# Kernel optimization log

Measured on AMD Instinct MI355X. Metric: run time of the kernel, lower is better.

## Reference

```python
import jax, jax.numpy as jnp
import numpy as np

EPS = 1e-9
NUM_CLASSES = 10


def setup_inputs() -> dict:
    key = jax.random.key(0)
    k1, k2, k3, k4 = jax.random.split(key, 4)
    B, N, D = 1024, 16384, 512
    bound = 1.0 / (D ** 0.5)
    return {
        "x": jax.random.normal(k1, (B, D), dtype=jnp.float32),
        "ex_feats": jax.random.normal(k2, (N, D), dtype=jnp.float32),
        "ex_labels": jax.random.randint(k3, (N,), 0, NUM_CLASSES),
        "w_unconstrained": jax.random.uniform(k4, (D,), dtype=jnp.float32, minval=-bound, maxval=bound),
        "gamma_unconstrained": jnp.asarray(1.0, dtype=jnp.float32),
        "beta_unconstrained": jnp.asarray(1.0, dtype=jnp.float32),
    }


def reference(x, ex_feats, ex_labels, w_unconstrained, gamma_unconstrained, beta_unconstrained):
    # Constrained parameters
    beta = jax.nn.softplus(beta_unconstrained) + EPS      # scalar
    gamma = jax.nn.softplus(gamma_unconstrained) + EPS    # scalar
    w = jax.nn.softmax(w_unconstrained) + EPS             # (D,), positive, ~sums to 1

    # Weighted squared distance via quadratic (GEMM) expansion:
    # d[b,n] = sum_k w_k * (x[b,k] - e[n,k])^2
    #        = (x^2 @ w)[b] + (e^2 @ w)[n] - 2 * ((x*w) @ e^T)[b,n]
    x2w = (x * x) @ w                                     # (B,)
    e2w = (ex_feats * ex_feats) @ w                       # (N,)
    cross = (x * w[None, :]) @ ex_feats.T                 # (B, N) GEMM
    d = x2w[:, None] + e2w[None, :] - 2.0 * cross         # (B, N)

    sim = jnp.exp(-beta * d)                              # (B, N)

    # Scatter-add sim by class label -> class_sum (B, C).
    # With small C this is a dense GEMM against a one-hot matrix.
    onehot = jax.nn.one_hot(ex_labels, NUM_CLASSES, dtype=sim.dtype)  # (N, C)
    class_sum = sim @ onehot                              # (B, C)

    logits = gamma * jnp.log(class_sum + EPS)
    return logits
```

## Files before the change

### kernel.cpp

```cpp
#include <hip/hip_runtime.h>
#include <hip/hip_bf16.h>
#include <cstdint>


typedef __attribute__((ext_vector_type(4))) float f32x4;
typedef __attribute__((ext_vector_type(8))) __bf16 bf16x8;
typedef __attribute__((ext_vector_type(4))) _Float16 half4;
typedef __attribute__((ext_vector_type(4))) unsigned int u32x4;

#define DDIM 512
#define NC 10
#define NCP 16
#define NECH 64
#define EPSF 1e-9f

__device__ inline float wave_sum(float v) {
  #pragma unroll
  for (int o = 32; o > 0; o >>= 1) v += __shfl_xor(v, o, 64);
  return v;
}

__device__ inline float softplus(float x) {
  return (x > 20.0f) ? x : log1pf(__expf(x));
}

__device__ inline unsigned cvtpk(float lo, float hi) {
  unsigned r;
  asm("v_cvt_pk_bf16_f32 %0, %1, %2" : "=v"(r) : "v"(lo), "v"(hi));
  return r;
}

__global__ __launch_bounds__(512, 2) void gemm_mega(
    const float* __restrict__ x, const float* __restrict__ ex,
    const int* __restrict__ labels, const float* __restrict__ wu,
    const float* __restrict__ bu, float* __restrict__ part) {
  __shared__ __attribute__((aligned(16))) unsigned short smem[2 * 16384];
  __shared__ float wlds[512];
  __shared__ float sm[16];
  __shared__ float e2l[256];
  __shared__ float x2l[256];
  __shared__ int lab[256];
  const int tid = threadIdx.x, lane = tid & 63, wid = tid >> 6;

  const int orig = blockIdx.x;
  const int xcd = orig & 7;
  const int local = orig >> 3;
  const int be = xcd * 8 + (local >> 2);
  const int bb = local & 3;

  if (tid < 256) lab[tid] = labels[be * 256 + tid];

  {
    float v = wu[tid];
    float m = v;
    #pragma unroll
    for (int o = 32; o > 0; o >>= 1) m = fmaxf(m, __shfl_xor(m, o, 64));
    if (lane == 0) sm[wid] = m;
    __syncthreads();
    float mm = sm[0];
    #pragma unroll
    for (int i = 1; i < 8; ++i) mm = fmaxf(mm, sm[i]);
    float e = __expf(v - mm);
    float s = wave_sum(e);
    if (lane == 0) sm[8 + wid] = s;
    __syncthreads();
    float ss = 0.f;
    #pragma unroll
    for (int i = 0; i < 8; ++i) ss += sm[8 + i];
    wlds[tid] = e / ss + EPSF;
    __syncthreads();
  }

  const int srow = tid >> 2;
  const int kc = (tid & 3) ^ (srow & 3);
  const float* eP0 = ex + (size_t)(be * 256 + srow) * DDIM + kc * 8;
  const float* eP1 = eP0 + (size_t)128 * DDIM;
  const float* xP0 = x + (size_t)(bb * 256 + srow) * DDIM + kc * 8;
  const float* xP1 = xP0 + (size_t)128 * DDIM;
  const int dE0 = tid * 8,           dE1 = (512 + tid) * 8;
  const int dX0 = 8192 + tid * 8,    dX1 = 8192 + (512 + tid) * 8;

  float e2a0 = 0.f, e2a1 = 0.f, x2a0 = 0.f, x2a1 = 0.f;

  const int WE = (wid >> 2) * 128;
  const int WB = (wid & 3) * 64;
  int eoff[8], xoff[4];
  {
    const int ch = lane >> 4;
    #pragma unroll
    for (int f = 0; f < 8; ++f) {
      int er = WE + f * 16 + (lane & 15);
      eoff[f] = er * 64 + ((ch ^ (er & 3)) * 16);
    }
    #pragma unroll
    for (int f = 0; f < 4; ++f) {
      int xr = WB + f * 16 + (lane & 15);
      xoff[f] = 16384 + xr * 64 + ((ch ^ (xr & 3)) * 16);
    }
  }

  float4 sE0a, sE0b, sE1a, sE1b, sX0a, sX0b, sX1a, sX1b;

#define ISSUE(KT) do {                                                  \
    const float* p0 = eP0 + (KT) * 32;                                  \
    const float* p1 = eP1 + (KT) * 32;                                  \
    const float* p2 = xP0 + (KT) * 32;                                  \
    const float* p3 = xP1 + (KT) * 32;                                  \
    sE0a = *(const float4*)p0; sE0b = *(const float4*)(p0 + 4);         \
    sE1a = *(const float4*)p1; sE1b = *(const float4*)(p1 + 4);         \
    sX0a = *(const float4*)p2; sX0b = *(const float4*)(p2 + 4);         \
    sX1a = *(const float4*)p3; sX1b = *(const float4*)(p3 + 4);         \
  } while (0)

#define CVTSTORE(KT, BUFS) do {                                         \
    const float4 w0 = *(const float4*)&wlds[(KT) * 32 + kc * 8];        \
    const float4 w1 = *(const float4*)&wlds[(KT) * 32 + kc * 8 + 4];    \
    u32x4 pk;                                                           \
    pk[0] = cvtpk(sE0a.x, sE0a.y); pk[1] = cvtpk(sE0a.z, sE0a.w);       \
    pk[2] = cvtpk(sE0b.x, sE0b.y); pk[3] = cvtpk(sE0b.z, sE0b.w);       \
    e2a0 += sE0a.x*sE0a.x*w0.x + sE0a.y*sE0a.y*w0.y                     \
          + sE0a.z*sE0a.z*w0.z + sE0a.w*sE0a.w*w0.w                     \
          + sE0b.x*sE0b.x*w1.x + sE0b.y*sE0b.y*w1.y                     \
          + sE0b.z*sE0b.z*w1.z + sE0b.w*sE0b.w*w1.w;                    \
    *(u32x4*)&smem[(BUFS) + dE0] = pk;                                  \
    pk[0] = cvtpk(sE1a.x, sE1a.y); pk[1] = cvtpk(sE1a.z, sE1a.w);       \
    pk[2] = cvtpk(sE1b.x, sE1b.y); pk[3] = cvtpk(sE1b.z, sE1b.w);       \
    e2a1 += sE1a.x*sE1a.x*w0.x + sE1a.y*sE1a.y*w0.y                     \
          + sE1a.z*sE1a.z*w0.z + sE1a.w*sE1a.w*w0.w                     \
          + sE1b.x*sE1b.x*w1.x + sE1b.y*sE1b.y*w1.y                     \
          + sE1b.z*sE1b.z*w1.z + sE1b.w*sE1b.w*w1.w;                    \
    *(u32x4*)&smem[(BUFS) + dE1] = pk;                                  \
    float a0 = sX0a.x*w0.x, a1 = sX0a.y*w0.y, a2 = sX0a.z*w0.z,         \
          a3 = sX0a.w*w0.w, a4 = sX0b.x*w1.x, a5 = sX0b.y*w1.y,         \
          a6 = sX0b.z*w1.z, a7 = sX0b.w*w1.w;                           \
    pk[0] = cvtpk(a0, a1); pk[1] = cvtpk(a2, a3);                       \
    pk[2] = cvtpk(a4, a5); pk[3] = cvtpk(a6, a7);                       \
    x2a0 += a0*sX0a.x + a1*sX0a.y + a2*sX0a.z + a3*sX0a.w               \
          + a4*sX0b.x + a5*sX0b.y + a6*sX0b.z + a7*sX0b.w;              \
    *(u32x4*)&smem[(BUFS) + dX0] = pk;                                  \
    a0 = sX1a.x*w0.x; a1 = sX1a.y*w0.y; a2 = sX1a.z*w0.z;               \
    a3 = sX1a.w*w0.w; a4 = sX1b.x*w1.x; a5 = sX1b.y*w1.y;               \
    a6 = sX1b.z*w1.z; a7 = sX1b.w*w1.w;                                 \
    pk[0] = cvtpk(a0, a1); pk[1] = cvtpk(a2, a3);                       \
    pk[2] = cvtpk(a4, a5); pk[3] = cvtpk(a6, a7);                       \
    x2a1 += a0*sX1a.x + a1*sX1a.y + a2*sX1a.z + a3*sX1a.w               \
          + a4*sX1b.x + a5*sX1b.y + a6*sX1b.z + a7*sX1b.w;              \
    *(u32x4*)&smem[(BUFS) + dX1] = pk;                                  \
  } while (0)

  ISSUE(0);
  CVTSTORE(0, 0);
  __syncthreads();

  f32x4 acc[8][4] = {};
  for (int kt = 0; kt < 16; ++kt) {
    const int cur = kt & 1;
    if (kt < 15) ISSUE(kt + 1);
    const char* base = (const char*)smem + cur * 32768;
    bf16x8 ef[8], xf[4];
    #pragma unroll
    for (int f = 0; f < 8; ++f) ef[f] = *(const bf16x8*)(base + eoff[f]);
    #pragma unroll
    for (int f = 0; f < 4; ++f) xf[f] = *(const bf16x8*)(base + xoff[f]);
    #pragma unroll
    for (int fe = 0; fe < 8; ++fe)
      #pragma unroll
      for (int fb = 0; fb < 4; ++fb)
        acc[fe][fb] = __builtin_amdgcn_mfma_f32_16x16x32_bf16(ef[fe], xf[fb], acc[fe][fb], 0, 0, 0);
    if (kt < 15) CVTSTORE(kt + 1, (cur ^ 1) * 16384);
    __syncthreads();
  }
#undef ISSUE
#undef CVTSTORE

  e2a0 += __shfl_xor(e2a0, 1, 64); e2a0 += __shfl_xor(e2a0, 2, 64);
  e2a1 += __shfl_xor(e2a1, 1, 64); e2a1 += __shfl_xor(e2a1, 2, 64);
  x2a0 += __shfl_xor(x2a0, 1, 64); x2a0 += __shfl_xor(x2a0, 2, 64);
  x2a1 += __shfl_xor(x2a1, 1, 64); x2a1 += __shfl_xor(x2a1, 2, 64);
  if ((tid & 3) == 0) {
    e2l[srow] = e2a0; e2l[srow + 128] = e2a1;
    x2l[srow] = x2a0; x2l[srow + 128] = x2a1;
  }
  __syncthreads();

  const float beta = softplus(bu[0]) + EPSF;
  const int rb = (lane >> 4) * 4;
  const int col = lane & 15;
  float e2v[8][4];
  #pragma unroll
  for (int fe = 0; fe < 8; ++fe)
    #pragma unroll
    for (int r = 0; r < 4; ++r)
      e2v[fe][r] = e2l[WE + fe * 16 + rb + r];
  half4 oh[8];
  #pragma unroll
  for (int fe = 0; fe < 8; ++fe)
    #pragma unroll
    for (int i = 0; i < 4; ++i)
      oh[fe][i] = (lab[WE + fe * 16 + rb + i] == col) ? (_Float16)1.0f : (_Float16)0.0f;

  f32x4 csv[4];
  #pragma unroll
  for (int fb = 0; fb < 4; ++fb) {
    const float xv = x2l[WB + fb * 16 + col];
    f32x4 cs = {0.f, 0.f, 0.f, 0.f};
    #pragma unroll
    for (int fe = 0; fe < 8; ++fe) {
      half4 sa;
      #pragma unroll
      for (int r = 0; r < 4; ++r)
        sa[r] = (_Float16)__expf(-beta * (xv + e2v[fe][r] - 2.0f * acc[fe][fb][r]));
      cs = __builtin_amdgcn_mfma_f32_16x16x16f16(sa, oh[fe], cs, 0, 0, 0);
    }
    csv[fb] = cs;
  }

  float* red = (float*)smem;
  const int half = WE >> 7;
  #pragma unroll
  for (int fb = 0; fb < 4; ++fb)
    #pragma unroll
    for (int r = 0; r < 4; ++r)
      red[(((half << 8) | (WB + fb * 16 + rb + r)) << 4) | col] = csv[fb][r];
  __syncthreads();

  {
    const int o = tid * 8;
    const int rl = o >> 4;
    const int c0 = o & 15;
    const float4* p0 = (const float4*)&red[(rl << 4) | c0];
    const float4* p1 = (const float4*)&red[((256 | rl) << 4) | c0];
    float4 a0 = p0[0], a1 = p0[1], b0 = p1[0], b1 = p1[1];
    float4 r0 = {a0.x + b0.x, a0.y + b0.y, a0.z + b0.z, a0.w + b0.w};
    float4 r1 = {a1.x + b1.x, a1.y + b1.y, a1.z + b1.z, a1.w + b1.w};
    float* g = &part[(((size_t)(bb * 256 + rl)) * NECH + be) * NCP + c0];
    *(float4*)g = r0;
    *(float4*)(g + 4) = r1;
  }
}

__global__ __launch_bounds__(256) void reduce_logits(
    const float* __restrict__ part, const float* __restrict__ gu,
    float* __restrict__ out) {
  const int lane = threadIdx.x & 63, wd = threadIdx.x >> 6;
  const int b = blockIdx.x * 4 + wd;
  const int cl = lane & 15, ch0 = lane >> 4;
  const float* p = part + (size_t)b * NECH * NCP;
  float v = 0.f;
  #pragma unroll
  for (int k = 0; k < 16; ++k)
    v += p[(ch0 + 4 * k) * NCP + cl];
  v += __shfl_xor(v, 16, 64);
  v += __shfl_xor(v, 32, 64);
  if (lane < NC) {
    const float gamma = softplus(gu[0]) + EPSF;
    out[b * NC + lane] = gamma * logf(v + EPSF);
  }
}

extern "C" void kernel_launch(void* const* d_in, const int* in_sizes, int n_in,
                              void* d_out, int out_size, void* d_ws, size_t ws_size,
                              hipStream_t stream) {
  const float* x  = (const float*)d_in[0];
  const float* ex = (const float*)d_in[1];
  const int* labels = (const int*)d_in[2];
  const float* wu = (const float*)d_in[3];
  const float* gu = (const float*)d_in[4];
  const float* bu = (const float*)d_in[5];
  float* out = (float*)d_out;
  const int B = in_sizes[0] / DDIM;
  const int N = in_sizes[2];

  float* part = (float*)d_ws;
  const size_t need = (size_t)B * NECH * NCP * 4;
  if (ws_size < need) return;

  gemm_mega<<<(N / 256) * (B / 256), 512, 0, stream>>>(x, ex, labels, wu, bu, part);
  reduce_logits<<<B / 4, 256, 0, stream>>>(part, gu, out);
}
```

Before: 39.94 us.

## Double block to 1024 threads and halve per-wave GEMM tile

Each block now runs 16 waves instead of 8. Each wave computes a 64x64 slice of the 256x256 tile instead of 128x64, and each thread stages one row chunk per operand instead of two. The aim is more latency hiding and lower per-thread register pressure. The LDS swizzle changes to XOR on (row>>1)&3. The final class-sum reduction now combines four partial quadrants instead of two. The launch bound of (1024,4) requests a very aggressive register budget, which may cause spills, and per-wave MFMA reuse of LDS fragments drops.

```diff
diff --git a/kernel.cpp b/kernel.cpp
--- a/kernel.cpp
+++ b/kernel.cpp
@@ -14,12 +14,6 @@
 #define NECH 64
 #define EPSF 1e-9f
 
-__device__ inline float wave_sum(float v) {
-  #pragma unroll
-  for (int o = 32; o > 0; o >>= 1) v += __shfl_xor(v, o, 64);
-  return v;
-}
-
 __device__ inline float softplus(float x) {
   return (x > 20.0f) ? x : log1pf(__expf(x));
 }
@@ -30,7 +24,7 @@
   return r;
 }
 
-__global__ __launch_bounds__(512, 2) void gemm_mega(
+__global__ __launch_bounds__(1024, 4) void gemm_mega(
     const float* __restrict__ x, const float* __restrict__ ex,
     const int* __restrict__ labels, const float* __restrict__ wu,
     const float* __restrict__ bu, float* __restrict__ part) {
@@ -50,7 +44,7 @@
 
   if (tid < 256) lab[tid] = labels[be * 256 + tid];
 
-  {
+  if (tid < 512) {
     float v = wu[tid];
     float m = v;
     #pragma unroll
@@ -61,109 +55,91 @@
     #pragma unroll
     for (int i = 1; i < 8; ++i) mm = fmaxf(mm, sm[i]);
     float e = __expf(v - mm);
-    float s = wave_sum(e);
+    float s = e;
+    #pragma unroll
+    for (int o = 32; o > 0; o >>= 1) s += __shfl_xor(s, o, 64);
     if (lane == 0) sm[8 + wid] = s;
     __syncthreads();
     float ss = 0.f;
     #pragma unroll
     for (int i = 0; i < 8; ++i) ss += sm[8 + i];
     wlds[tid] = e / ss + EPSF;
-    __syncthreads();
-  }
+  } else {
+    __syncthreads();
+    __syncthreads();
+  }
+  __syncthreads();
 
   const int srow = tid >> 2;
-  const int kc = (tid & 3) ^ (srow & 3);
-  const float* eP0 = ex + (size_t)(be * 256 + srow) * DDIM + kc * 8;
-  const float* eP1 = eP0 + (size_t)128 * DDIM;
-  const float* xP0 = x + (size_t)(bb * 256 + srow) * DDIM + kc * 8;
-  const float* xP1 = xP0 + (size_t)128 * DDIM;
-  const int dE0 = tid * 8,           dE1 = (512 + tid) * 8;
-  const int dX0 = 8192 + tid * 8,    dX1 = 8192 + (512 + tid) * 8;
-
-  float e2a0 = 0.f, e2a1 = 0.f, x2a0 = 0.f, x2a1 = 0.f;
-
-  const int WE = (wid >> 2) * 128;
+  const int kc = (tid & 3) ^ ((srow >> 1) & 3);
+  const float* eP = ex + (size_t)(be * 256 + srow) * DDIM + kc * 8;
+  const float* xP = x + (size_t)(bb * 256 + srow) * DDIM + kc * 8;
+  const int dE = tid * 8;
+  const int dX = 8192 + tid * 8;
+
+  float e2a = 0.f, x2a = 0.f;
+
+  const int WE = (wid >> 2) * 64;
   const int WB = (wid & 3) * 64;
-  int eoff[8], xoff[4];
+  int eoff[4], xoff[4];
   {
     const int ch = lane >> 4;
     #pragma unroll
-    for (int f = 0; f < 8; ++f) {
+    for (int f = 0; f < 4; ++f) {
       int er = WE + f * 16 + (lane & 15);
-      eoff[f] = er * 64 + ((ch ^ (er & 3)) * 16);
+      eoff[f] = er * 64 + ((ch ^ ((er >> 1) & 3)) * 16);
+      int xr = WB + f * 16 + (lane & 15);
+      xoff[f] = 16384 + xr * 64 + ((ch ^ ((xr >> 1) & 3)) * 16);
     }
-    #pragma unroll
-    for (int f = 0; f < 4; ++f) {
-      int xr = WB + f * 16 + (lane & 15);
-      xoff[f] = 16384 + xr * 64 + ((ch ^ (xr & 3)) * 16);
-    }
-  }
-
-  float4 sE0a, sE0b, sE1a, sE1b, sX0a, sX0b, sX1a, sX1b;
+  }
+
+  float4 sEa, sEb, sXa, sXb;
 
 #define ISSUE(KT) do {                                                  \
-    const float* p0 = eP0 + (KT) * 32;                                  \
-    const float* p1 = eP1 + (KT) * 32;                                  \
-    const float* p2 = xP0 + (KT) * 32;                                  \
-    const float* p3 = xP1 + (KT) * 32;                                  \
-    sE0a = *(const float4*)p0; sE0b = *(const float4*)(p0 + 4);         \
-    sE1a = *(const float4*)p1; sE1b = *(const float4*)(p1 + 4);         \
-    sX0a = *(const float4*)p2; sX0b = *(const float4*)(p2 + 4);         \
-    sX1a = *(const float4*)p3; sX1b = *(const float4*)(p3 + 4);         \
+    const float* p0 = eP + (KT) * 32;                                   \
+    const float* p1 = xP + (KT) * 32;                                   \
+    sEa = *(const float4*)p0; sEb = *(const float4*)(p0 + 4);           \
+    sXa = *(const float4*)p1; sXb = *(const float4*)(p1 + 4);           \
   } while (0)
 
 #define CVTSTORE(KT, BUFS) do {                                         \
     const float4 w0 = *(const float4*)&wlds[(KT) * 32 + kc * 8];        \
     const float4 w1 = *(const float4*)&wlds[(KT) * 32 + kc * 8 + 4];    \
     u32x4 pk;                                                           \
-    pk[0] = cvtpk(sE0a.x, sE0a.y); pk[1] = cvtpk(sE0a.z, sE0a.w);       \
-    pk[2] = cvtpk(sE0b.x, sE0b.y); pk[3] = cvtpk(sE0b.z, sE0b.w);       \
-    e2a0 += sE0a.x*sE0a.x*w0.x + sE0a.y*sE0a.y*w0.y                     \
-          + sE0a.z*sE0a.z*w0.z + sE0a.w*sE0a.w*w0.w                     \
-          + sE0b.x*sE0b.x*w1.x + sE0b.y*sE0b.y*w1.y                     \
-          + sE0b.z*sE0b.z*w1.z + sE0b.w*sE0b.w*w1.w;                    \
-    *(u32x4*)&smem[(BUFS) + dE0] = pk;                                  \
-    pk[0] = cvtpk(sE1a.x, sE1a.y); pk[1] = cvtpk(sE1a.z, sE1a.w);       \
-    pk[2] = cvtpk(sE1b.x, sE1b.y); pk[3] = cvtpk(sE1b.z, sE1b.w);       \
-    e2a1 += sE1a.x*sE1a.x*w0.x + sE1a.y*sE1a.y*w0.y                     \
-          + sE1a.z*sE1a.z*w0.z + sE1a.w*sE1a.w*w0.w                     \
-          + sE1b.x*sE1b.x*w1.x + sE1b.y*sE1b.y*w1.y                     \
-          + sE1b.z*sE1b.z*w1.z + sE1b.w*sE1b.w*w1.w;                    \
-    *(u32x4*)&smem[(BUFS) + dE1] = pk;                                  \
-    float a0 = sX0a.x*w0.x, a1 = sX0a.y*w0.y, a2 = sX0a.z*w0.z,         \
-          a3 = sX0a.w*w0.w, a4 = sX0b.x*w1.x, a5 = sX0b.y*w1.y,         \
-          a6 = sX0b.z*w1.z, a7 = sX0b.w*w1.w;                           \
+    pk[0] = cvtpk(sEa.x, sEa.y); pk[1] = cvtpk(sEa.z, sEa.w);           \
+    pk[2] = cvtpk(sEb.x, sEb.y); pk[3] = cvtpk(sEb.z, sEb.w);           \
+    e2a += sEa.x*sEa.x*w0.x + sEa.y*sEa.y*w0.y                          \
+         + sEa.z*sEa.z*w0.z + sEa.w*sEa.w*w0.w                          \
+         + sEb.x*sEb.x*w1.x + sEb.y*sEb.y*w1.y                          \
+         + sEb.z*sEb.z*w1.z + sEb.w*sEb.w*w1.w;                         \
+    *(u32x4*)&smem[(BUFS) + dE] = pk;                                   \
+    float a0 = sXa.x*w0.x, a1 = sXa.y*w0.y, a2 = sXa.z*w0.z,            \
+          a3 = sXa.w*w0.w, a4 = sXb.x*w1.x, a5 = sXb.y*w1.y,            \
+          a6 = sXb.z*w1.z, a7 = sXb.w*w1.w;                             \
     pk[0] = cvtpk(a0, a1); pk[1] = cvtpk(a2, a3);                       \
     pk[2] = cvtpk(a4, a5); pk[3] = cvtpk(a6, a7);                       \
-    x2a0 += a0*sX0a.x + a1*sX0a.y + a2*sX0a.z + a3*sX0a.w               \
-          + a4*sX0b.x + a5*sX0b.y + a6*sX0b.z + a7*sX0b.w;              \
-    *(u32x4*)&smem[(BUFS) + dX0] = pk;                                  \
-    a0 = sX1a.x*w0.x; a1 = sX1a.y*w0.y; a2 = sX1a.z*w0.z;               \
-    a3 = sX1a.w*w0.w; a4 = sX1b.x*w1.x; a5 = sX1b.y*w1.y;               \
-    a6 = sX1b.z*w1.z; a7 = sX1b.w*w1.w;                                 \
-    pk[0] = cvtpk(a0, a1); pk[1] = cvtpk(a2, a3);                       \
-    pk[2] = cvtpk(a4, a5); pk[3] = cvtpk(a6, a7);                       \
-    x2a1 += a0*sX1a.x + a1*sX1a.y + a2*sX1a.z + a3*sX1a.w               \
-          + a4*sX1b.x + a5*sX1b.y + a6*sX1b.z + a7*sX1b.w;              \
-    *(u32x4*)&smem[(BUFS) + dX1] = pk;                                  \
+    x2a += a0*sXa.x + a1*sXa.y + a2*sXa.z + a3*sXa.w                    \
+         + a4*sXb.x + a5*sXb.y + a6*sXb.z + a7*sXb.w;                   \
+    *(u32x4*)&smem[(BUFS) + dX] = pk;                                   \
   } while (0)
 
   ISSUE(0);
   CVTSTORE(0, 0);
   __syncthreads();
 
-  f32x4 acc[8][4] = {};
+  f32x4 acc[4][4] = {};
   for (int kt = 0; kt < 16; ++kt) {
     const int cur = kt & 1;
     if (kt < 15) ISSUE(kt + 1);
     const char* base = (const char*)smem + cur * 32768;
-    bf16x8 ef[8], xf[4];
-    #pragma unroll
-    for (int f = 0; f < 8; ++f) ef[f] = *(const bf16x8*)(base + eoff[f]);
-    #pragma unroll
-    for (int f = 0; f < 4; ++f) xf[f] = *(const bf16x8*)(base + xoff[f]);
-    #pragma unroll
-    for (int fe = 0; fe < 8; ++fe)
+    bf16x8 ef[4], xf[4];
+    #pragma unroll
+    for (int f = 0; f < 4; ++f) {
+      ef[f] = *(const bf16x8*)(base + eoff[f]);
+      xf[f] = *(const bf16x8*)(base + xoff[f]);
+    }
+    #pragma unroll
+    for (int fe = 0; fe < 4; ++fe)
       #pragma unroll
       for (int fb = 0; fb < 4; ++fb)
         acc[fe][fb] = __builtin_amdgcn_mfma_f32_16x16x32_bf16(ef[fe], xf[fb], acc[fe][fb], 0, 0, 0);
@@ -173,28 +149,26 @@
 #undef ISSUE
 #undef CVTSTORE
 
-  e2a0 += __shfl_xor(e2a0, 1, 64); e2a0 += __shfl_xor(e2a0, 2, 64);
-  e2a1 += __shfl_xor(e2a1, 1, 64); e2a1 += __shfl_xor(e2a1, 2, 64);
-  x2a0 += __shfl_xor(x2a0, 1, 64); x2a0 += __shfl_xor(x2a0, 2, 64);
-  x2a1 += __shfl_xor(x2a1, 1, 64); x2a1 += __shfl_xor(x2a1, 2, 64);
+  e2a += __shfl_xor(e2a, 1, 64); e2a += __shfl_xor(e2a, 2, 64);
+  x2a += __shfl_xor(x2a, 1, 64); x2a += __shfl_xor(x2a, 2, 64);
   if ((tid & 3) == 0) {
-    e2l[srow] = e2a0; e2l[srow + 128] = e2a1;
-    x2l[srow] = x2a0; x2l[srow + 128] = x2a1;
+    e2l[srow] = e2a;
+    x2l[srow] = x2a;
   }
   __syncthreads();
 
   const float beta = softplus(bu[0]) + EPSF;
   const int rb = (lane >> 4) * 4;
   const int col = lane & 15;
-  float e2v[8][4];
-  #pragma unroll
-  for (int fe = 0; fe < 8; ++fe)
+  float e2v[4][4];
+  #pragma unroll
+  for (int fe = 0; fe < 4; ++fe)
     #pragma unroll
     for (int r = 0; r < 4; ++r)
       e2v[fe][r] = e2l[WE + fe * 16 + rb + r];
-  half4 oh[8];
-  #pragma unroll
-  for (int fe = 0; fe < 8; ++fe)
+  half4 oh[4];
+  #pragma unroll
+  for (int fe = 0; fe < 4; ++fe)
     #pragma unroll
     for (int i = 0; i < 4; ++i)
       oh[fe][i] = (lab[WE + fe * 16 + rb + i] == col) ? (_Float16)1.0f : (_Float16)0.0f;
@@ -205,7 +179,7 @@
     const float xv = x2l[WB + fb * 16 + col];
     f32x4 cs = {0.f, 0.f, 0.f, 0.f};
     #pragma unroll
-    for (int fe = 0; fe < 8; ++fe) {
+    for (int fe = 0; fe < 4; ++fe) {
       half4 sa;
       #pragma unroll
       for (int r = 0; r < 4; ++r)
@@ -216,26 +190,25 @@
   }
 
   float* red = (float*)smem;
-  const int half = WE >> 7;
+  const int quad = WE >> 6;
   #pragma unroll
   for (int fb = 0; fb < 4; ++fb)
     #pragma unroll
     for (int r = 0; r < 4; ++r)
-      red[(((half << 8) | (WB + fb * 16 + rb + r)) << 4) | col] = csv[fb][r];
+      red[((quad * 256 + (WB + fb * 16 + rb + r)) << 4) | col] = csv[fb][r];
   __syncthreads();
 
   {
-    const int o = tid * 8;
+    const int o = tid * 4;
     const int rl = o >> 4;
-    const int c0 = o & 15;
-    const float4* p0 = (const float4*)&red[(rl << 4) | c0];
-    const float4* p1 = (const float4*)&red[((256 | rl) << 4) | c0];
-    float4 a0 = p0[0], a1 = p0[1], b0 = p1[0], b1 = p1[1];
-    float4 r0 = {a0.x + b0.x, a0.y + b0.y, a0.z + b0.z, a0.w + b0.w};
-    float4 r1 = {a1.x + b1.x, a1.y + b1.y, a1.z + b1.z, a1.w + b1.w};
-    float* g = &part[(((size_t)(bb * 256 + rl)) * NECH + be) * NCP + c0];
-    *(float4*)g = r0;
-    *(float4*)(g + 4) = r1;
+    const int c0 = o & 12;
+    float4 v0 = *(const float4*)&red[(rl << 4) | c0];
+    float4 v1 = *(const float4*)&red[((256 + rl) << 4) | c0];
+    float4 v2 = *(const float4*)&red[((512 + rl) << 4) | c0];
+    float4 v3 = *(const float4*)&red[((768 + rl) << 4) | c0];
+    float4 r0 = {v0.x + v1.x + v2.x + v3.x, v0.y + v1.y + v2.y + v3.y,
+                 v0.z + v1.z + v2.z + v3.z, v0.w + v1.w + v2.w + v3.w};
+    *(float4*)&part[(((size_t)(bb * 256 + rl)) * NECH + be) * NCP + c0] = r0;
   }
 }
 
@@ -275,6 +248,6 @@
   const size_t need = (size_t)B * NECH * NCP * 4;
   if (ws_size < need) return;
 
-  gemm_mega<<<(N / 256) * (B / 256), 512, 0, stream>>>(x, ex, labels, wu, bu, part);
+  gemm_mega<<<(N / 256) * (B / 256), 1024, 0, stream>>>(x, ex, labels, wu, bu, part);
   reduce_logits<<<B / 4, 256, 0, stream>>>(part, gu, out);
 }
```

Result: faster. 38.08 us (median of 2 runs) (-4.7%).
